# Optimization experiments

Hardware: AMD Instinct MI355X
Metric: run time of the kernel (lower is better)

## Reference

```python
import math
import jax, jax.numpy as jnp
import numpy as np

# ---- static hyperparams (match init_kwargs) ----
B, D, K, NC, F = 16384, 64, 128, 64, 256
TAU_MIN = 0.01
TAU_DENOM_MIN = 0.001
EPS = 0.001  # transport_eps


def setup_inputs() -> dict:
    key = jax.random.key(0)
    ks = jax.random.split(key, 8)
    # latent positions strictly inside the Poincare ball (norm < 0.9)
    z = jax.random.normal(ks[0], (B, D), jnp.float32)
    z = z / (jnp.linalg.norm(z, axis=-1, keepdims=True) + 1e-6)
    z = z * (0.9 * jax.random.uniform(ks[1], (B, 1), jnp.float32))
    features = jax.random.normal(ks[2], (B, F), jnp.float32)
    q_z_w = jax.random.normal(ks[3], (K, D), jnp.float32) * 0.02
    q_z_b = jnp.zeros((K,), jnp.float32)
    q_feat_w = jax.random.normal(ks[4], (K, F), jnp.float32) * 0.02
    q_feat_b = jnp.zeros((K,), jnp.float32)
    q_gamma = jax.random.normal(ks[5], (K, D, D), jnp.float32) * 0.02
    chart_queries = jax.random.normal(ks[6], (NC, K), jnp.float32) * 0.02
    return {"z": z, "features": features, "q_z_w": q_z_w, "q_z_b": q_z_b,
            "q_feat_w": q_feat_w, "q_feat_b": q_feat_b, "q_gamma": q_gamma,
            "chart_queries": chart_queries}


def _hyperbolic_score(z, centers):
    # z: [B, D]; centers: [NC, D] -> scores [B, NC]
    diff = z[:, None, :] - centers[None, :, :]
    dist_sq = (diff ** 2).sum(-1)                       # [B, NC]
    z_sq = (z ** 2).sum(-1, keepdims=True)              # [B, 1]
    c_sq = (centers ** 2).sum(-1)[None, :]              # [1, NC]
    denom = (1.0 - z_sq) * (1.0 - c_sq)
    arg = 1.0 + 2.0 * dist_sq / (denom + EPS)
    dist = jnp.arccosh(jnp.maximum(arg, 1.0 + EPS))
    # metric-aware temperature tau(z)
    tau = math.sqrt(K) * jnp.maximum(1.0 - z_sq[:, 0], TAU_DENOM_MIN) / 2.0
    tau = jnp.maximum(tau, TAU_MIN)                     # [B]
    return -dist / tau[:, None]


def reference(z, features, q_z_w, q_z_b, q_feat_w, q_feat_b, q_gamma, chart_queries):
    # chart centers live in the first D coords of the chart queries
    centers = chart_queries[:, :D]                      # [NC, D]
    scores = _hyperbolic_score(z, centers)              # [B, NC]

    # query: linear(z) + linear(features) + bilinear gamma term
    q = z @ q_z_w.T + q_z_b + features @ q_feat_w.T + q_feat_b   # [B, K]
    q = q + jnp.einsum("bi,bj,kij->bk", z, z, q_gamma)           # gamma contraction

    # O(n) hyperbolic parallel transport: scale queries by 1/lambda(z)
    r2 = jnp.minimum((z ** 2).sum(-1, keepdims=True), 1.0 - EPS)  # [B, 1]
    lam = 2.0 / (1.0 - r2 + EPS)                                  # [B, 1]
    tq = chart_queries[None, :, :] / lam[:, None, :]              # [B, NC, K]

    scores = scores + jnp.einsum("bk,bnk->bn", q, tq) / math.sqrt(K)
    weights = jax.nn.softmax(scores, axis=-1)           # [B, NC] (soft routing)
    k_chart = jnp.argmax(weights, axis=-1)              # [B]
    return weights, k_chart
```

## Files before the change

### kernel.cpp

```cpp
#include <hip/hip_runtime.h>
#include <hip/hip_bf16.h>
#include <cmath>
#include <cstring>

#define B_TOT 16384

typedef unsigned int uint_t;
typedef unsigned short ushort_t;
typedef __attribute__((ext_vector_type(8))) short bf16x8;
typedef __attribute__((ext_vector_type(16))) float f32x16;

#define WS_TAB 0
#define WS_CSQ 1024
#define WS_LIN 4096
#define WS_S   4198400
#define WS_PPK 5246976

__global__ __launch_bounds__(256) void prep_s(const float* __restrict__ g,
                                              const float* __restrict__ cq,
                                              char* __restrict__ ws) {
  __shared__ float gl[128][68];
  __shared__ float cql[16][132];
  float* S = (float*)(ws + WS_S);
  const int ns = blockIdx.x >> 6, J = blockIdx.x & 63, t = threadIdx.x;
  for (int i = t; i < 2048; i += 256) {
    const int k = i >> 4, c4 = (i & 15) * 4;
    *(float4*)&gl[k][c4] = *(const float4*)(g + (size_t)k * 4096 + J * 64 + c4);
  }
  for (int i = t; i < 2048; i += 256) {
    const int n16 = i >> 7, k = i & 127;
    cql[n16][k] = cq[(ns * 16 + n16) * 128 + k];
  }
  __syncthreads();
  const int n16 = t >> 4, c4 = (t & 15) * 4;
  float4 acc = {0.f, 0.f, 0.f, 0.f};
#pragma unroll 8
  for (int k = 0; k < 128; ++k) {
    const float w = cql[n16][k];
    const float4 gv = *(const float4*)&gl[k][c4];
    acc.x = fmaf(w, gv.x, acc.x);
    acc.y = fmaf(w, gv.y, acc.y);
    acc.z = fmaf(w, gv.z, acc.z);
    acc.w = fmaf(w, gv.w, acc.w);
  }
  *(float4*)(S + (size_t)(ns * 16 + n16) * 4096 + J * 64 + c4) = acc;
}

__global__ __launch_bounds__(256) void prep_pack(
    const float* __restrict__ qfw, const float* __restrict__ cq,
    const float* __restrict__ qzw, const float* __restrict__ qzb,
    const float* __restrict__ qfb, char* __restrict__ ws) {
  __shared__ float Sl[4096];
  __shared__ uint_t tabl[192];
  __shared__ float psumf[128][2];
  const int n = blockIdx.x & 63, part = blockIdx.x >> 6, t = threadIdx.x;
  const float* __restrict__ S = (const float*)(ws + WS_S) + (size_t)n * 4096;
  for (int i = t; i < 4096; i += 256) Sl[i] = S[i];
  if (t < 64) {
    const int i = t;
    const int start = (i < 16) ? 4 * i
                     : (i < 32) ? 64 + 3 * (i - 16)
                     : (i < 48) ? 112 + 2 * (i - 32)
                                : 144 + (i - 48);
    const int nst = 4 - (i >> 4);
    for (int u = 0; u < nst; ++u)
      tabl[start + u] = (0u << 16) | ((uint_t)i << 8) | (uint_t)(16 * ((i >> 4) + u));
  } else if (t < 80) tabl[160 + (t - 64)] = (1u << 16) | (uint_t)((t - 64) * 16);
  else if (t < 84)   tabl[176 + (t - 80)] = (2u << 16) | (uint_t)((t - 80) * 16);
  else if (t == 84)  tabl[180] = (3u << 16);
  else if (t < 96)   tabl[181 + (t - 85)] = 0;
  __syncthreads();
  if (part == 0 && n == 0 && t < 192) ((uint_t*)(ws + WS_TAB))[t] = tabl[t];

  const int mt = n >> 5, r = n & 31;
  auto wpack = [&](int s, int jo, float val) {
    const __hip_bfloat16 hb = __float2bfloat16(val);
    const float hf = __bfloat162float(hb);
    const __hip_bfloat16 lb = __float2bfloat16(val - hf);
    ushort_t hu, lu;
    memcpy(&hu, &hb, 2);
    memcpy(&lu, &lb, 2);
    const size_t base =
        (((size_t)s * 4 + mt * 2) * 64 + ((jo >> 3) & 1) * 32 + r) * 16 + (jo & 7) * 2;
    *(ushort_t*)(ws + WS_PPK + base) = hu;
    *(ushort_t*)(ws + WS_PPK + base + 1024) = lu;
  };

  for (int v = part * 640 + t; v < (part + 1) * 640; v += 256) {
    const int s = v >> 4, jo = v & 15;
    const uint_t inf = tabl[s];
    const int i = (inf >> 8) & 255, j0 = inf & 255;
    const int j = j0 + jo;
    const float val =
        (j < i) ? 0.f : ((j > i) ? Sl[i * 64 + j] + Sl[j * 64 + i] : Sl[i * 64 + i]);
    wpack(s, jo, val);
  }
  const float* __restrict__ cqn = cq + n * 128;

  if (part >= 2) {
    const int fl = t & 127, kh = t >> 7;
    const int f = (part - 2) * 128 + fl;
    float a = 0.f;
#pragma unroll 8
    for (int k = 0; k < 64; ++k)
      a = fmaf(qfw[(kh * 64 + k) * 256 + f], cqn[kh * 64 + k], a);
    psumf[fl][kh] = a;
    __syncthreads();
    if (t < 128) {
      const int ff = (part - 2) * 128 + t;
      wpack(160 + (ff >> 4), ff & 15, psumf[t][0] + psumf[t][1]);
    }
  } else if (part == 1) {
    if (t < 64) {
      float a = 0.f;
#pragma unroll 8
      for (int k = 0; k < 128; ++k) a = fmaf(cqn[k], qzw[k * 64 + t], a);
      wpack(176 + (t >> 4), t & 15, a);
    }
    for (int v2 = t; v2 < 176; v2 += 256) wpack(181 + (v2 >> 4), v2 & 15, 0.f);
  } else {
    if (t == 128) {
      float a = 0.f;
      for (int k = 0; k < 128; ++k) a = fmaf(qzb[k] + qfb[k], cqn[k], a);
      wpack(180, 0, a);
    } else if (t > 128 && t < 144) wpack(180, t - 128, 0.f);
    if (t == 144) {
      double a = 0.0;
      for (int d = 0; d < 64; ++d) a = fma((double)cqn[d], (double)cqn[d], a);
      ((double*)(ws + WS_CSQ))[n] = a;
    }
  }
}

__global__ __launch_bounds__(256, 5) void gemm_kernel(
    const float* __restrict__ z, const float* __restrict__ feat,
    char* __restrict__ ws) {
  __shared__ __align__(16) unsigned char smem[17024];
  float (*z_lds)[68] = (float (*)[68])(smem);
  float (*s_lin)[65] = (float (*)[65])(smem + 8704);

  const int t = threadIdx.x, lane = t & 63;
  const int wv = __builtin_amdgcn_readfirstlane(t >> 6);
  const int b0 = blockIdx.x * 32;
  const int h = lane >> 5, c = lane & 31;

  for (int i = t; i < 2048; i += 256) z_lds[i >> 6][i & 63] = z[(size_t)b0 * 64 + i];
  if (t < 128) z_lds[t >> 2][64 + (t & 3)] = 0.f;
  for (int i = t; i < 32 * 65; i += 256) ((float*)s_lin)[i] = 0.f;
  __syncthreads();

  const bf16x8* __restrict__ pp = (const bf16x8*)(ws + WS_PPK);
  const uint_t* __restrict__ tab = (const uint_t*)(ws + WS_TAB);
  f32x16 acc[2] = {};
#pragma unroll 2
  for (int it = 0; it < 48; ++it) {
    const int s = wv + it * 4;
    const uint_t inf = tab[s];
    const int mode = inf >> 16, i_idx = (inf >> 8) & 255, p0 = inf & 255;
    const bf16x8 Ah0 = pp[((size_t)s * 4 + 0) * 64 + lane];
    const bf16x8 Al0 = pp[((size_t)s * 4 + 1) * 64 + lane];
    const bf16x8 Ah1 = pp[((size_t)s * 4 + 2) * 64 + lane];
    const bf16x8 Al1 = pp[((size_t)s * 4 + 3) * 64 + lane];
    const int bl = c;
    float xv[8];
    if (mode == 0) {
      const float zi = z_lds[bl][i_idx];
      const float* __restrict__ zp = &z_lds[bl][p0 + h * 8];
      const float4 a = *(const float4*)zp, b2 = *(const float4*)(zp + 4);
      xv[0] = zi * a.x; xv[1] = zi * a.y; xv[2] = zi * a.z; xv[3] = zi * a.w;
      xv[4] = zi * b2.x; xv[5] = zi * b2.y; xv[6] = zi * b2.z; xv[7] = zi * b2.w;
    } else if (mode == 1) {
      const float* __restrict__ fp = feat + (size_t)(b0 + bl) * 256 + p0 + h * 8;
      const float4 a = *(const float4*)fp, b2 = *(const float4*)(fp + 4);
      xv[0] = a.x; xv[1] = a.y; xv[2] = a.z; xv[3] = a.w;
      xv[4] = b2.x; xv[5] = b2.y; xv[6] = b2.z; xv[7] = b2.w;
    } else if (mode == 2) {
      const float* __restrict__ zp = &z_lds[bl][p0 + h * 8];
      const float4 a = *(const float4*)zp, b2 = *(const float4*)(zp + 4);
      xv[0] = a.x; xv[1] = a.y; xv[2] = a.z; xv[3] = a.w;
      xv[4] = b2.x; xv[5] = b2.y; xv[6] = b2.z; xv[7] = b2.w;
    } else {
      xv[0] = (h == 0) ? 1.f : 0.f;
      xv[1] = xv[2] = xv[3] = xv[4] = xv[5] = xv[6] = xv[7] = 0.f;
    }
    uint_t bhw[4], blw[4];
#pragma unroll
    for (int e2 = 0; e2 < 4; ++e2) {
      const float2 xp = {xv[2 * e2], xv[2 * e2 + 1]};
      const __hip_bfloat162 hb2 = __float22bfloat162_rn(xp);
      uint_t hw;
      memcpy(&hw, &hb2, 4);
      const float h0 = __uint_as_float(hw << 16);
      const float h1 = __uint_as_float(hw & 0xffff0000u);
      const float2 lp = {xp.x - h0, xp.y - h1};
      const __hip_bfloat162 lb2 = __float22bfloat162_rn(lp);
      uint_t lw;
      memcpy(&lw, &lb2, 4);
      bhw[e2] = hw;
      blw[e2] = lw;
    }
    bf16x8 Bh, Bl;
    memcpy(&Bh, bhw, 16);
    memcpy(&Bl, blw, 16);
    acc[0] = __builtin_amdgcn_mfma_f32_32x32x16_bf16(Ah0, Bh, acc[0], 0, 0, 0);
    acc[0] = __builtin_amdgcn_mfma_f32_32x32x16_bf16(Ah0, Bl, acc[0], 0, 0, 0);
    acc[0] = __builtin_amdgcn_mfma_f32_32x32x16_bf16(Al0, Bh, acc[0], 0, 0, 0);
    acc[1] = __builtin_amdgcn_mfma_f32_32x32x16_bf16(Ah1, Bh, acc[1], 0, 0, 0);
    acc[1] = __builtin_amdgcn_mfma_f32_32x32x16_bf16(Ah1, Bl, acc[1], 0, 0, 0);
    acc[1] = __builtin_amdgcn_mfma_f32_32x32x16_bf16(Al1, Bh, acc[1], 0, 0, 0);
  }
#pragma unroll
  for (int mt = 0; mt < 2; ++mt)
#pragma unroll
    for (int r = 0; r < 16; ++r) {
      const int n = mt * 32 + (r & 3) + 8 * (r >> 2) + 4 * h;
      atomicAdd(&s_lin[c][n], acc[mt][r]);
    }
  __syncthreads();
  float* __restrict__ gl = (float*)(ws + WS_LIN) + (size_t)b0 * 64;
  for (int i = t; i < 2048; i += 256) gl[i] = s_lin[i >> 6][i & 63];
}

__global__ __launch_bounds__(256, 4) void tail_kernel(
    const float* __restrict__ z, const float* __restrict__ cq,
    const char* __restrict__ ws, float* __restrict__ out) {
  __shared__ __align__(16) unsigned char smem[37504];
  float (*zt)[33] = (float (*)[33])(smem);
  float (*slin)[65] = (float (*)[65])(smem + 8448);
  float (*cqT)[65] = (float (*)[65])(smem + 16768);
  double (*s_exp)[65] = (double (*)[65])(smem + 16768);
  double (*pmax)[9] = (double (*)[9])(smem + 33408);
  int (*parg)[9] = (int (*)[9])(smem + 35712);
  double* rowmax = (double*)(smem + 36864);
  int* rowarg = (int*)(smem + 37120);
  double* rowinv = (double*)(smem + 37248);

  const int t = threadIdx.x;
  const int r = t & 31, cg = t >> 5;
  const int b0 = blockIdx.x * 32;

  for (int i = t; i < 2048; i += 256) zt[i & 63][i >> 6] = z[(size_t)b0 * 64 + i];
  for (int i = t; i < 2048; i += 256)
    slin[i >> 6][i & 63] = ((const float*)(ws + WS_LIN))[(size_t)b0 * 64 + i];
  for (int i = t; i < 4096; i += 256) {
    const int n = i >> 6, ii = i & 63;
    cqT[ii][n] = cq[n * 128 + ii];
  }
  __syncthreads();

  double z_sq = 0.0, zc[8] = {0.0, 0.0, 0.0, 0.0, 0.0, 0.0, 0.0, 0.0};
#pragma unroll 4
  for (int i = 0; i < 64; ++i) {
    const double zv = (double)zt[i][r];
    z_sq = fma(zv, zv, z_sq);
#pragma unroll
    for (int u = 0; u < 8; ++u)
      zc[u] = fma(zv, (double)cqT[i][cg + 8 * u], zc[u]);
  }
  float lin[8];
#pragma unroll
  for (int u = 0; u < 8; ++u) lin[u] = slin[r][cg + 8 * u];

  const double EPS = 0.001;
  const double SQRTK = sqrt(128.0);
  double tau = SQRTK * fmax(1.0 - z_sq, 0.001) * 0.5;
  tau = fmax(tau, 0.01);
  const double inv_tau = 1.0 / tau;
  const double r2 = fmin(z_sq, 1.0 - EPS);
  const double lam_fac = (1.0 - r2 + EPS) * 0.5 / SQRTK;
  const double* __restrict__ csqd = (const double*)(ws + WS_CSQ);

  double sc[8];
#pragma unroll
  for (int u = 0; u < 8; ++u) {
    const int n = cg + 8 * u;
    const double c_sq = csqd[n];
    const double dist_sq = z_sq + c_sq - 2.0 * zc[u];
    const double denom = (1.0 - z_sq) * (1.0 - c_sq);
    double arg = 1.0 + 2.0 * dist_sq / (denom + EPS);
    arg = fmax(arg, 1.0 + EPS);
    const double dist = log(arg + sqrt(arg * arg - 1.0));
    sc[u] = -dist * inv_tau + (double)lin[u] * lam_fac;
  }
  __syncthreads();

  {
    double mx = sc[0];
    int am = cg;
#pragma unroll
    for (int u = 1; u < 8; ++u)
      if (sc[u] > mx) { mx = sc[u]; am = cg + 8 * u; }
    pmax[r][cg] = mx;
    parg[r][cg] = am;
  }
  __syncthreads();
  if (t < 32) {
    double m = pmax[t][0];
    int a = parg[t][0];
#pragma unroll
    for (int g = 1; g < 8; ++g) {
      const double v = pmax[t][g];
      const int aa = parg[t][g];
      if (v > m || (v == m && aa < a)) { m = v; a = aa; }
    }
    rowmax[t] = m;
    rowarg[t] = a;
  }
  __syncthreads();
  {
    const double m = rowmax[r];
    double ps = 0.0;
#pragma unroll
    for (int u = 0; u < 8; ++u) {
      const double e = exp(sc[u] - m);
      s_exp[r][cg + 8 * u] = e;
      ps += e;
    }
    pmax[r][cg] = ps;
  }
  __syncthreads();
  if (t < 32) {
    double s = 0.0;
#pragma unroll
    for (int g = 0; g < 8; ++g) s += pmax[t][g];
    rowinv[t] = 1.0 / s;
  }
  __syncthreads();
  for (int idx = t; idx < 2048; idx += 256) {
    const int b = idx >> 6, n = idx & 63;
    out[(size_t)(b0 + b) * 64 + n] = (float)(s_exp[b][n] * rowinv[b]);
  }
  if (t < 32) out[(size_t)B_TOT * 64 + b0 + t] = (float)rowarg[t];
}

extern "C" void kernel_launch(void* const* d_in, const int* in_sizes, int n_in,
                              void* d_out, int out_size, void* d_ws, size_t ws_size,
                              hipStream_t stream) {
  const float* z = (const float*)d_in[0];
  const float* feat = (const float*)d_in[1];
  const float* qzw = (const float*)d_in[2];
  const float* qzb = (const float*)d_in[3];
  const float* qfw = (const float*)d_in[4];
  const float* qfb = (const float*)d_in[5];
  const float* gamma = (const float*)d_in[6];
  const float* cq = (const float*)d_in[7];
  float* out = (float*)d_out;
  char* ws = (char*)d_ws;

  prep_s<<<dim3(256), dim3(256), 0, stream>>>(gamma, cq, ws);
  prep_pack<<<dim3(256), dim3(256), 0, stream>>>(qfw, cq, qzw, qzb, qfb, ws);
  gemm_kernel<<<dim3(B_TOT / 32), dim3(256), 0, stream>>>(z, feat, ws);
  tail_kernel<<<dim3(B_TOT / 32), dim3(256), 0, stream>>>(z, cq, ws, out);
}
```

Measured before the change: 158.3 us.

## Split GEMM K-dimension across two blocks and halve tail block rows

Result: slower. 176.7 us (+11.6%).

```diff
diff --git a/kernel.cpp b/kernel.cpp
--- a/kernel.cpp
+++ b/kernel.cpp
@@ -13,8 +13,20 @@
 #define WS_TAB 0
 #define WS_CSQ 1024
 #define WS_LIN 4096
-#define WS_S   4198400
-#define WS_PPK 5246976
+#define WS_S   8392704
+#define WS_PPK 9441280
+#define LIN_HALF (B_TOT * 64)
+
+__device__ __forceinline__ void decode_step(int s, int& mode, int& i_idx, int& p0) {
+  if (s < 64) { mode = 0; i_idx = s >> 2; p0 = (s & 3) * 16; }
+  else if (s < 112) { const int q = s - 64, qd = q / 3; mode = 0; i_idx = 16 + qd; p0 = 16 * (1 + (q - 3 * qd)); }
+  else if (s < 144) { const int q = s - 112; mode = 0; i_idx = 32 + (q >> 1); p0 = 16 * (2 + (q & 1)); }
+  else if (s < 160) { mode = 0; i_idx = 48 + (s - 144); p0 = 48; }
+  else if (s < 176) { mode = 1; i_idx = 0; p0 = (s - 160) * 16; }
+  else if (s < 180) { mode = 2; i_idx = 0; p0 = (s - 176) * 16; }
+  else if (s == 180) { mode = 3; i_idx = 0; p0 = 0; }
+  else { mode = 2; i_idx = 0; p0 = 0; }
+}
 
 __global__ __launch_bounds__(256) void prep_s(const float* __restrict__ g,
                                               const float* __restrict__ cq,
@@ -141,7 +153,8 @@
 
   const int t = threadIdx.x, lane = t & 63;
   const int wv = __builtin_amdgcn_readfirstlane(t >> 6);
-  const int b0 = blockIdx.x * 32;
+  const int ksl = blockIdx.x & 1;
+  const int b0 = (blockIdx.x >> 1) * 32;
   const int h = lane >> 5, c = lane & 31;
 
   for (int i = t; i < 2048; i += 256) z_lds[i >> 6][i & 63] = z[(size_t)b0 * 64 + i];
@@ -150,13 +163,12 @@
   __syncthreads();
 
   const bf16x8* __restrict__ pp = (const bf16x8*)(ws + WS_PPK);
-  const uint_t* __restrict__ tab = (const uint_t*)(ws + WS_TAB);
   f32x16 acc[2] = {};
 #pragma unroll 2
-  for (int it = 0; it < 48; ++it) {
-    const int s = wv + it * 4;
-    const uint_t inf = tab[s];
-    const int mode = inf >> 16, i_idx = (inf >> 8) & 255, p0 = inf & 255;
+  for (int it = 0; it < 24; ++it) {
+    const int s = ksl * 4 + wv + it * 8;
+    int mode, i_idx, p0;
+    decode_step(s, mode, i_idx, p0);
     const bf16x8 Ah0 = pp[((size_t)s * 4 + 0) * 64 + lane];
     const bf16x8 Al0 = pp[((size_t)s * 4 + 1) * 64 + lane];
     const bf16x8 Ah1 = pp[((size_t)s * 4 + 2) * 64 + lane];
@@ -217,49 +229,53 @@
       atomicAdd(&s_lin[c][n], acc[mt][r]);
     }
   __syncthreads();
-  float* __restrict__ gl = (float*)(ws + WS_LIN) + (size_t)b0 * 64;
+  float* __restrict__ gl =
+      (float*)(ws + WS_LIN) + (size_t)ksl * LIN_HALF + (size_t)b0 * 64;
   for (int i = t; i < 2048; i += 256) gl[i] = s_lin[i >> 6][i & 63];
 }
 
 __global__ __launch_bounds__(256, 4) void tail_kernel(
     const float* __restrict__ z, const float* __restrict__ cq,
     const char* __restrict__ ws, float* __restrict__ out) {
-  __shared__ __align__(16) unsigned char smem[37504];
-  float (*zt)[33] = (float (*)[33])(smem);
-  float (*slin)[65] = (float (*)[65])(smem + 8448);
-  float (*cqT)[65] = (float (*)[65])(smem + 16768);
-  double (*s_exp)[65] = (double (*)[65])(smem + 16768);
-  double (*pmax)[9] = (double (*)[9])(smem + 33408);
-  int (*parg)[9] = (int (*)[9])(smem + 35712);
-  double* rowmax = (double*)(smem + 36864);
-  int* rowarg = (int*)(smem + 37120);
-  double* rowinv = (double*)(smem + 37248);
+  __shared__ __align__(16) unsigned char smem[28736];
+  float (*zt)[17] = (float (*)[17])(smem);
+  float (*slin)[65] = (float (*)[65])(smem + 4352);
+  float (*cqT)[65] = (float (*)[65])(smem + 8512);
+  double (*s_exp)[65] = (double (*)[65])(smem + 8512);
+  double (*pmax)[17] = (double (*)[17])(smem + 25152);
+  int (*parg)[17] = (int (*)[17])(smem + 27328);
+  double* rowmax = (double*)(smem + 28416);
+  int* rowarg = (int*)(smem + 28544);
+  double* rowinv = (double*)(smem + 28608);
 
   const int t = threadIdx.x;
-  const int r = t & 31, cg = t >> 5;
-  const int b0 = blockIdx.x * 32;
-
-  for (int i = t; i < 2048; i += 256) zt[i & 63][i >> 6] = z[(size_t)b0 * 64 + i];
-  for (int i = t; i < 2048; i += 256)
-    slin[i >> 6][i & 63] = ((const float*)(ws + WS_LIN))[(size_t)b0 * 64 + i];
+  const int r = t & 15, cg = t >> 4;
+  const int b0 = blockIdx.x * 16;
+  const float* __restrict__ l0 = (const float*)(ws + WS_LIN) + (size_t)b0 * 64;
+  const float* __restrict__ l1 = l0 + LIN_HALF;
+
+  for (int i = t; i < 1024; i += 256) {
+    zt[i & 63][i >> 6] = z[(size_t)b0 * 64 + i];
+    slin[i >> 6][i & 63] = l0[i] + l1[i];
+  }
   for (int i = t; i < 4096; i += 256) {
     const int n = i >> 6, ii = i & 63;
     cqT[ii][n] = cq[n * 128 + ii];
   }
   __syncthreads();
 
-  double z_sq = 0.0, zc[8] = {0.0, 0.0, 0.0, 0.0, 0.0, 0.0, 0.0, 0.0};
-#pragma unroll 4
+  double z_sq = 0.0, zc[4] = {0.0, 0.0, 0.0, 0.0};
+#pragma unroll 8
   for (int i = 0; i < 64; ++i) {
     const double zv = (double)zt[i][r];
     z_sq = fma(zv, zv, z_sq);
 #pragma unroll
-    for (int u = 0; u < 8; ++u)
-      zc[u] = fma(zv, (double)cqT[i][cg + 8 * u], zc[u]);
-  }
-  float lin[8];
-#pragma unroll
-  for (int u = 0; u < 8; ++u) lin[u] = slin[r][cg + 8 * u];
+    for (int u = 0; u < 4; ++u)
+      zc[u] = fma(zv, (double)cqT[i][cg + 16 * u], zc[u]);
+  }
+  float lin[4];
+#pragma unroll
+  for (int u = 0; u < 4; ++u) lin[u] = slin[r][cg + 16 * u];
 
   const double EPS = 0.001;
   const double SQRTK = sqrt(128.0);
@@ -270,10 +286,10 @@
   const double lam_fac = (1.0 - r2 + EPS) * 0.5 / SQRTK;
   const double* __restrict__ csqd = (const double*)(ws + WS_CSQ);
 
-  double sc[8];
-#pragma unroll
-  for (int u = 0; u < 8; ++u) {
-    const int n = cg + 8 * u;
+  double sc[4];
+#pragma unroll
+  for (int u = 0; u < 4; ++u) {
+    const int n = cg + 16 * u;
     const double c_sq = csqd[n];
     const double dist_sq = z_sq + c_sq - 2.0 * zc[u];
     const double denom = (1.0 - z_sq) * (1.0 - c_sq);
@@ -288,17 +304,17 @@
     double mx = sc[0];
     int am = cg;
 #pragma unroll
-    for (int u = 1; u < 8; ++u)
-      if (sc[u] > mx) { mx = sc[u]; am = cg + 8 * u; }
+    for (int u = 1; u < 4; ++u)
+      if (sc[u] > mx) { mx = sc[u]; am = cg + 16 * u; }
     pmax[r][cg] = mx;
     parg[r][cg] = am;
   }
   __syncthreads();
-  if (t < 32) {
+  if (t < 16) {
     double m = pmax[t][0];
     int a = parg[t][0];
 #pragma unroll
-    for (int g = 1; g < 8; ++g) {
+    for (int g = 1; g < 16; ++g) {
       const double v = pmax[t][g];
       const int aa = parg[t][g];
       if (v > m || (v == m && aa < a)) { m = v; a = aa; }
@@ -311,26 +327,26 @@
     const double m = rowmax[r];
     double ps = 0.0;
 #pragma unroll
-    for (int u = 0; u < 8; ++u) {
+    for (int u = 0; u < 4; ++u) {
       const double e = exp(sc[u] - m);
-      s_exp[r][cg + 8 * u] = e;
+      s_exp[r][cg + 16 * u] = e;
       ps += e;
     }
     pmax[r][cg] = ps;
   }
   __syncthreads();
-  if (t < 32) {
+  if (t < 16) {
     double s = 0.0;
 #pragma unroll
-    for (int g = 0; g < 8; ++g) s += pmax[t][g];
+    for (int g = 0; g < 16; ++g) s += pmax[t][g];
     rowinv[t] = 1.0 / s;
   }
   __syncthreads();
-  for (int idx = t; idx < 2048; idx += 256) {
+  for (int idx = t; idx < 1024; idx += 256) {
     const int b = idx >> 6, n = idx & 63;
     out[(size_t)(b0 + b) * 64 + n] = (float)(s_exp[b][n] * rowinv[b]);
   }
-  if (t < 32) out[(size_t)B_TOT * 64 + b0 + t] = (float)rowarg[t];
+  if (t < 16) out[(size_t)B_TOT * 64 + b0 + t] = (float)rowarg[t];
 }
 
 extern "C" void kernel_launch(void* const* d_in, const int* in_sizes, int n_in,
@@ -349,6 +365,6 @@
 
   prep_s<<<dim3(256), dim3(256), 0, stream>>>(gamma, cq, ws);
   prep_pack<<<dim3(256), dim3(256), 0, stream>>>(qfw, cq, qzw, qzb, qfb, ws);
-  gemm_kernel<<<dim3(B_TOT / 32), dim3(256), 0, stream>>>(z, feat, ws);
-  tail_kernel<<<dim3(B_TOT / 32), dim3(256), 0, stream>>>(z, cq, ws, out);
-}
+  gemm_kernel<<<dim3(1024), dim3(256), 0, stream>>>(z, feat, ws);
+  tail_kernel<<<dim3(1024), dim3(256), 0, stream>>>(z, cq, ws, out);
+}
```
